# Performance work log

Measured on AMD Instinct MI355X. Metric: run time of the kernel, lower is better.

## Reference

```python
import jax, jax.numpy as jnp
import numpy as np

ENT_TYPES = 9
INNER_DIM = 64


def setup_inputs() -> dict:
    key = jax.random.key(0)
    k1, k2 = jax.random.split(key)
    B, S, H = 8, 1024, 768
    last_hidden_state = jax.random.normal(k1, (B, S, H), dtype=jnp.float32)
    attention_mask = jnp.ones((B, S), dtype=jnp.float32)
    dense_w = jax.random.normal(k2, (ENT_TYPES * INNER_DIM * 2, H), dtype=jnp.float32) * (1.0 / np.sqrt(H))
    dense_b = jnp.zeros((ENT_TYPES * INNER_DIM * 2,), dtype=jnp.float32)
    return {
        "last_hidden_state": last_hidden_state,
        "attention_mask": attention_mask,
        "dense_w": dense_w,
        "dense_b": dense_b,
    }


def _sinusoidal_pos_emb(seq_len: int, output_dim: int, dtype):
    # (seq_len, output_dim) interleaved as [sin0, cos0, sin1, cos1, ...]
    position = jnp.arange(seq_len, dtype=dtype)[:, None]              # (S, 1)
    indices = jnp.arange(output_dim // 2, dtype=dtype)
    inv_freq = jnp.power(jnp.asarray(10000.0, dtype), -2.0 * indices / output_dim)
    ang = position * inv_freq                                         # (S, D/2)
    emb = jnp.stack([jnp.sin(ang), jnp.cos(ang)], axis=-1)            # (S, D/2, 2)
    return emb.reshape(seq_len, output_dim)


def reference(last_hidden_state, attention_mask, dense_w, dense_b):
    B, S, H = last_hidden_state.shape
    D = INNER_DIM
    E = ENT_TYPES

    # dense projection then split into per-entity-type q/k of width D each
    out = last_hidden_state @ dense_w.T + dense_b                     # (B, S, 2*E*D)
    out = out.reshape(B, S, E, 2 * D)                                 # (B, S, E, 2D)
    qw, kw = out[..., :D], out[..., D:]                               # (B, S, E, D)

    # RoPE: duplicated cos/sin pairs, half-rotation
    pos = _sinusoidal_pos_emb(S, D, last_hidden_state.dtype)          # (S, D)
    cos_pos = jnp.repeat(pos[:, 1::2], 2, axis=-1)[None, :, None, :]  # (1, S, 1, D)
    sin_pos = jnp.repeat(pos[:, 0::2], 2, axis=-1)[None, :, None, :]

    def rotate_half(x):
        x1, x2 = x[..., : D // 2], x[..., D // 2 :]
        return jnp.concatenate([-x2, x1], axis=-1)

    qw = qw * cos_pos + rotate_half(qw) * sin_pos
    kw = kw * cos_pos + rotate_half(kw) * sin_pos

    # pairwise entity scores
    logits = jnp.einsum("bmhd,bnhd->bhmn", qw, kw) / jnp.sqrt(jnp.asarray(D, logits_dtype := last_hidden_state.dtype))

    # padding mask along key axis (as in original)
    pad_mask = attention_mask[:, None, None, :]                       # (B, 1, 1, S)
    logits = logits * pad_mask - (1.0 - pad_mask) * 10000.0

    # upper-triangular validity mask (start <= end)
    tri = jnp.triu(jnp.ones((S, S), dtype=logits.dtype))[None, None]  # (1, 1, S, S)
    logits = logits - (1.0 - tri) * 10000.0
    return logits
```

## Files before the change

### kernel.cpp

```cpp
#include <hip/hip_runtime.h>

#define BB 8
#define SS 1024
#define HH 768
#define EE 9
#define DD 64
#define NCOL (EE * 2 * DD)

typedef __bf16 bf16x8 __attribute__((ext_vector_type(8)));
typedef float f32x4 __attribute__((ext_vector_type(4)));

__device__ __forceinline__ unsigned short f2b(float f) {
    unsigned int x = __float_as_uint(f);
    unsigned int r = (x + 0x7fffu + ((x >> 16) & 1u)) >> 16;
    return (unsigned short)r;
}

__device__ __forceinline__ void gload_lds16(const void* g, void* l) {
    __builtin_amdgcn_global_load_lds(
        (const __attribute__((address_space(1))) void*)g,
        (__attribute__((address_space(3))) void*)l, 16, 0, 0);
}

__global__ __launch_bounds__(256) void to_bf16(const float* __restrict__ in,
                                               unsigned short* __restrict__ out,
                                               int n4) {
    int i = blockIdx.x * 256 + threadIdx.x;
    if (i >= n4) return;
    float4 v = ((const float4*)in)[i];
    ushort4 o = {f2b(v.x), f2b(v.y), f2b(v.z), f2b(v.w)};
    ((ushort4*)out)[i] = o;
}

__global__ __launch_bounds__(256) void dense_rope_mfma(
    const unsigned short* __restrict__ Abf,
    const unsigned short* __restrict__ Wbf,
    const float* __restrict__ bias,
    unsigned short* __restrict__ q_ws,
    unsigned short* __restrict__ k_ws) {
    __shared__ unsigned short As[128 * 32];
    __shared__ unsigned short Bs[128 * 32];

    const int t = threadIdx.x;
    const int lane = t & 63, wave = t >> 6;
    const int quad = lane >> 4, lr = lane & 15;
    const int wm = wave >> 1, wn = wave & 1;
    const int j0 = blockIdx.x * 128;
    const int m0 = blockIdx.y * 128;

    f32x4 acc[4][4] = {};

    const int srow = wave * 16 + (lane >> 2);
    const int sc8 = (lane & 3) * 8;

    for (int kt = 0; kt < HH / 32; ++kt) {
        const int k0 = kt * 32;
        __syncthreads();
#pragma unroll
        for (int i = 0; i < 2; ++i) {
            const int row = i * 64 + srow;
            const int lb = i * 2048 + wave * 512;
            gload_lds16(&Abf[(size_t)(m0 + row) * HH + k0 + sc8], &As[lb]);
            gload_lds16(&Wbf[(size_t)(j0 + row) * HH + k0 + sc8], &Bs[lb]);
        }
        __syncthreads();

        bf16x8 af[4], bf[4];
#pragma unroll
        for (int nt = 0; nt < 4; ++nt)
            af[nt] = *(const bf16x8*)&Bs[(wn * 64 + nt * 16 + lr) * 32 + quad * 8];
#pragma unroll
        for (int st = 0; st < 4; ++st)
            bf[st] = *(const bf16x8*)&As[(wm * 64 + st * 16 + lr) * 32 + quad * 8];
#pragma unroll
        for (int nt = 0; nt < 4; ++nt)
#pragma unroll
            for (int st = 0; st < 4; ++st)
                acc[nt][st] = __builtin_amdgcn_mfma_f32_16x16x32_bf16(
                    af[nt], bf[st], acc[nt][st], 0, 0, 0);
    }

    const int gcol0 = j0 + wn * 64;
    const int g = gcol0 >> 6;
    const int e = g >> 1;
    unsigned short* dst = (g & 1) ? k_ws : q_ws;
    const int b_idx = m0 >> 10;
    const size_t zbase = (size_t)(b_idx * EE + e) * SS;
    const float L2C = 0.4152410118609203f;

    float4 bb[4];
    float iv0[4], iv1[4];
#pragma unroll
    for (int nt = 0; nt < 4; ++nt) {
        bb[nt] = *(const float4*)&bias[gcol0 + nt * 16 + quad * 4];
        const int h0 = nt * 8 + quad * 2;
        iv0[nt] = exp2f(-(float)h0 * L2C);
        iv1[nt] = exp2f(-(float)(h0 + 1) * L2C);
    }
    const int s0 = (m0 & (SS - 1)) + wm * 64;
#pragma unroll
    for (int st = 0; st < 4; ++st) {
        const int s = s0 + st * 16 + lr;
        const float sf = (float)s;
        float c[4][4];
#pragma unroll
        for (int nt = 0; nt < 4; ++nt) {
            c[nt][0] = acc[nt][st][0] + bb[nt].x;
            c[nt][1] = acc[nt][st][1] + bb[nt].y;
            c[nt][2] = acc[nt][st][2] + bb[nt].z;
            c[nt][3] = acc[nt][st][3] + bb[nt].w;
        }
        unsigned short* drow = &dst[(zbase + s) * DD + quad * 4];
#pragma unroll
        for (int nt = 0; nt < 4; ++nt) {
            float sv0, cv0, sv1, cv1;
            __sincosf(sf * iv0[nt], &sv0, &cv0);
            __sincosf(sf * iv1[nt], &sv1, &cv1);
            float r0 = (nt < 2) ? -c[nt + 2][0] : c[nt - 2][0];
            float r1 = (nt < 2) ? -c[nt + 2][1] : c[nt - 2][1];
            float r2 = (nt < 2) ? -c[nt + 2][2] : c[nt - 2][2];
            float r3 = (nt < 2) ? -c[nt + 2][3] : c[nt - 2][3];
            ushort4 o = {f2b(c[nt][0] * cv0 + r0 * sv0),
                         f2b(c[nt][1] * cv0 + r1 * sv0),
                         f2b(c[nt][2] * cv1 + r2 * sv1),
                         f2b(c[nt][3] * cv1 + r3 * sv1)};
            *(ushort4*)&drow[nt * 16] = o;
        }
    }
}

#define LDA2 72
__global__ __launch_bounds__(256) void logits_mfma(
    const unsigned short* __restrict__ q_ws,
    const unsigned short* __restrict__ k_ws,
    const float* __restrict__ mask,
    float* __restrict__ out) {
    __shared__ unsigned short Qs[128 * LDA2];
    __shared__ unsigned short Ks[128 * LDA2];

    const int t = threadIdx.x;
    const int lane = t & 63, wave = t >> 6;
    const int quad = lane >> 4, lr = lane & 15;
    const int wm = wave >> 1, wn = wave & 1;
    const int n0 = blockIdx.x * 128;
    const int m0 = blockIdx.y * 128;
    const int z = blockIdx.z;
    const int b_idx = z / EE;

    const uint4* qsrc = (const uint4*)(q_ws + ((size_t)z * SS + m0) * DD);
    const uint4* ksrc = (const uint4*)(k_ws + ((size_t)z * SS + n0) * DD);
#pragma unroll
    for (int i = 0; i < 4; ++i) {
        int idx = t + i * 256;
        int row = idx >> 3, c8 = (idx & 7) * 8;
        uint4 qv = qsrc[idx];
        uint4 kv = ksrc[idx];
        *(uint4*)&Qs[row * LDA2 + c8] = qv;
        *(uint4*)&Ks[row * LDA2 + c8] = kv;
    }
    __syncthreads();

    f32x4 acc[4][4] = {};
#pragma unroll
    for (int ks = 0; ks < DD; ks += 32) {
        bf16x8 af[4], bf[4];
#pragma unroll
        for (int nt = 0; nt < 4; ++nt)
            af[nt] = *(const bf16x8*)&Ks[(wn * 64 + nt * 16 + lr) * LDA2 + ks + quad * 8];
#pragma unroll
        for (int mt = 0; mt < 4; ++mt)
            bf[mt] = *(const bf16x8*)&Qs[(wm * 64 + mt * 16 + lr) * LDA2 + ks + quad * 8];
#pragma unroll
        for (int nt = 0; nt < 4; ++nt)
#pragma unroll
            for (int mt = 0; mt < 4; ++mt)
                acc[nt][mt] = __builtin_amdgcn_mfma_f32_16x16x32_bf16(
                    af[nt], bf[mt], acc[nt][mt], 0, 0, 0);
    }

    const int nb0 = n0 + wn * 64;
    float4 pv[4];
#pragma unroll
    for (int nt = 0; nt < 4; ++nt)
        pv[nt] = *(const float4*)&mask[b_idx * SS + nb0 + nt * 16 + quad * 4];

    float* outz = out + (size_t)z * SS * SS;
#pragma unroll
    for (int mt = 0; mt < 4; ++mt) {
        const int m = m0 + wm * 64 + mt * 16 + lr;
        float* rowp = &outz[(size_t)m * SS];
#pragma unroll
        for (int nt = 0; nt < 4; ++nt) {
            const int nb = nb0 + nt * 16 + quad * 4;
            f32x4 v;
#pragma unroll
            for (int reg = 0; reg < 4; ++reg) {
                const float p = (&pv[nt].x)[reg];
                float x = acc[nt][mt][reg] * 0.125f;
                x = x * p - (1.0f - p) * 10000.0f;
                if (nb + reg < m) x -= 10000.0f;
                v[reg] = x;
            }
            __builtin_nontemporal_store(v, (f32x4*)(rowp + nb));
        }
    }
}

extern "C" void kernel_launch(void* const* d_in, const int* in_sizes, int n_in,
                              void* d_out, int out_size, void* d_ws, size_t ws_size,
                              hipStream_t stream) {
    const float* lhs  = (const float*)d_in[0];
    const float* mask = (const float*)d_in[1];
    const float* W    = (const float*)d_in[2];
    const float* bias = (const float*)d_in[3];
    float* out = (float*)d_out;

    unsigned short* q_ws = (unsigned short*)d_ws;
    unsigned short* k_ws = q_ws + (size_t)BB * EE * SS * DD;
    unsigned short* Abf  = k_ws + (size_t)BB * EE * SS * DD;
    unsigned short* Wbf  = Abf + (size_t)BB * SS * HH;

    to_bf16<<<(BB * SS * HH) / 4 / 256, 256, 0, stream>>>(lhs, Abf, (BB * SS * HH) / 4);
    to_bf16<<<(NCOL * HH) / 4 / 256, 256, 0, stream>>>(W, Wbf, (NCOL * HH) / 4);

    dim3 g1(NCOL / 128, (BB * SS) / 128);
    dense_rope_mfma<<<g1, 256, 0, stream>>>(Abf, Wbf, bias, q_ws, k_ws);

    dim3 g2(SS / 128, SS / 128, BB * EE);
    logits_mfma<<<g2, 256, 0, stream>>>(q_ws, k_ws, mask, out);
}
```

Measured before the change: 388.1 us.

## Load logits operands directly to registers, merge bf16 conversions, drop nontemporal stores

The logits kernel now reads Q and K fragments straight from global memory into registers instead of staging them through LDS behind a barrier, which frees shared memory and removes the sync. The two fp32-to-bf16 conversion launches become a single kernel, saving one launch. The output stores switch from nontemporal to ordinary stores. Direct global fragment loads are less coalesced (16-byte pieces strided by rows), and the ordinary stores may pollute the cache for the large output.

After: 383.0 us. No clear change (-1.3%).

```diff
diff --git a/kernel.cpp b/kernel.cpp
--- a/kernel.cpp
+++ b/kernel.cpp
@@ -22,14 +22,25 @@
         (__attribute__((address_space(3))) void*)l, 16, 0, 0);
 }
 
-__global__ __launch_bounds__(256) void to_bf16(const float* __restrict__ in,
-                                               unsigned short* __restrict__ out,
-                                               int n4) {
+__global__ __launch_bounds__(256) void to_bf16_2(
+    const float* __restrict__ a, int n4a,
+    const float* __restrict__ w, int n4w,
+    unsigned short* __restrict__ oa,
+    unsigned short* __restrict__ ow) {
     int i = blockIdx.x * 256 + threadIdx.x;
-    if (i >= n4) return;
-    float4 v = ((const float4*)in)[i];
+    const float* src;
+    unsigned short* dst;
+    int j;
+    if (i < n4a) {
+        src = a; dst = oa; j = i;
+    } else {
+        j = i - n4a;
+        if (j >= n4w) return;
+        src = w; dst = ow;
+    }
+    float4 v = ((const float4*)src)[j];
     ushort4 o = {f2b(v.x), f2b(v.y), f2b(v.z), f2b(v.w)};
-    ((ushort4*)out)[i] = o;
+    ((ushort4*)dst)[j] = o;
 }
 
 __global__ __launch_bounds__(256) void dense_rope_mfma(
@@ -129,15 +140,11 @@
     }
 }
 
-#define LDA2 72
 __global__ __launch_bounds__(256) void logits_mfma(
     const unsigned short* __restrict__ q_ws,
     const unsigned short* __restrict__ k_ws,
     const float* __restrict__ mask,
     float* __restrict__ out) {
-    __shared__ unsigned short Qs[128 * LDA2];
-    __shared__ unsigned short Ks[128 * LDA2];
-
     const int t = threadIdx.x;
     const int lane = t & 63, wave = t >> 6;
     const int quad = lane >> 4, lr = lane & 15;
@@ -147,36 +154,29 @@
     const int z = blockIdx.z;
     const int b_idx = z / EE;
 
-    const uint4* qsrc = (const uint4*)(q_ws + ((size_t)z * SS + m0) * DD);
-    const uint4* ksrc = (const uint4*)(k_ws + ((size_t)z * SS + n0) * DD);
-#pragma unroll
-    for (int i = 0; i < 4; ++i) {
-        int idx = t + i * 256;
-        int row = idx >> 3, c8 = (idx & 7) * 8;
-        uint4 qv = qsrc[idx];
-        uint4 kv = ksrc[idx];
-        *(uint4*)&Qs[row * LDA2 + c8] = qv;
-        *(uint4*)&Ks[row * LDA2 + c8] = kv;
-    }
-    __syncthreads();
+    const unsigned short* kb =
+        k_ws + ((size_t)z * SS + n0 + wn * 64 + lr) * DD + quad * 8;
+    const unsigned short* qb =
+        q_ws + ((size_t)z * SS + m0 + wm * 64 + lr) * DD + quad * 8;
+
+    bf16x8 af[2][4], bf[2][4];
+#pragma unroll
+    for (int x = 0; x < 4; ++x) {
+        af[0][x] = *(const bf16x8*)&kb[(size_t)(x * 16) * DD];
+        af[1][x] = *(const bf16x8*)&kb[(size_t)(x * 16) * DD + 32];
+        bf[0][x] = *(const bf16x8*)&qb[(size_t)(x * 16) * DD];
+        bf[1][x] = *(const bf16x8*)&qb[(size_t)(x * 16) * DD + 32];
+    }
 
     f32x4 acc[4][4] = {};
 #pragma unroll
-    for (int ks = 0; ks < DD; ks += 32) {
-        bf16x8 af[4], bf[4];
-#pragma unroll
-        for (int nt = 0; nt < 4; ++nt)
-            af[nt] = *(const bf16x8*)&Ks[(wn * 64 + nt * 16 + lr) * LDA2 + ks + quad * 8];
-#pragma unroll
-        for (int mt = 0; mt < 4; ++mt)
-            bf[mt] = *(const bf16x8*)&Qs[(wm * 64 + mt * 16 + lr) * LDA2 + ks + quad * 8];
+    for (int ks = 0; ks < 2; ++ks)
 #pragma unroll
         for (int nt = 0; nt < 4; ++nt)
 #pragma unroll
             for (int mt = 0; mt < 4; ++mt)
                 acc[nt][mt] = __builtin_amdgcn_mfma_f32_16x16x32_bf16(
-                    af[nt], bf[mt], acc[nt][mt], 0, 0, 0);
-    }
+                    af[ks][nt], bf[ks][mt], acc[nt][mt], 0, 0, 0);
 
     const int nb0 = n0 + wn * 64;
     float4 pv[4];
@@ -201,7 +201,7 @@
                 if (nb + reg < m) x -= 10000.0f;
                 v[reg] = x;
             }
-            __builtin_nontemporal_store(v, (f32x4*)(rowp + nb));
+            *(f32x4*)(rowp + nb) = v;
         }
     }
 }
@@ -220,8 +220,10 @@
     unsigned short* Abf  = k_ws + (size_t)BB * EE * SS * DD;
     unsigned short* Wbf  = Abf + (size_t)BB * SS * HH;
 
-    to_bf16<<<(BB * SS * HH) / 4 / 256, 256, 0, stream>>>(lhs, Abf, (BB * SS * HH) / 4);
-    to_bf16<<<(NCOL * HH) / 4 / 256, 256, 0, stream>>>(W, Wbf, (NCOL * HH) / 4);
+    const int n4a = (BB * SS * HH) / 4;
+    const int n4w = (NCOL * HH) / 4;
+    const int nconv = (n4a + n4w + 255) / 256;
+    to_bf16_2<<<nconv, 256, 0, stream>>>(lhs, n4a, W, n4w, Abf, Wbf);
 
     dim3 g1(NCOL / 128, (BB * SS) / 128);
     dense_rope_mfma<<<g1, 256, 0, stream>>>(Abf, Wbf, bias, q_ws, k_ws);
```
